# Optimization experiments

Hardware: AMD Instinct MI355X
Metric: run time of the kernel (lower is better)

The kernel has to match this reference:

```python
import jax, jax.numpy as jnp
from jax import lax
import numpy as np

N_STEPS = 5  # hard-coded truncated history length in the module


def setup_inputs() -> dict:
    key = jax.random.key(0)
    kH, kv, k1, k2, k3 = jax.random.split(key, 5)
    B, S, D = 32, 512, 512
    scale = 1.0 / np.sqrt(D)  # keep tanh/softmax out of saturation
    return {
        "H": jax.random.normal(kH, (B, S, D), dtype=jnp.float32),
        "v": jax.random.normal(kv, (D, 1), dtype=jnp.float32) * scale,
        "W1": jax.random.normal(k1, (D, D), dtype=jnp.float32) * scale,
        "W2": jax.random.normal(k2, (D, D), dtype=jnp.float32) * scale,
        "W3": jax.random.normal(k3, (D, D), dtype=jnp.float32) * scale,
    }


def reference(H, v, W1, W2, W3):
    # H: [B, S, D] -> output [B, S, D] (torch returns list of S tensors [B,1,D])
    B, S, D = H.shape

    def step(carry, ht):  # ht: [B, D]
        H_prev, H_prev_tilde = carry  # each [B, N_STEPS, D]
        # temp: [B, N_STEPS, D]; ht @ W2 broadcasts over the history axis
        temp = jnp.tanh(H_prev @ W1 + (ht @ W2)[:, None, :] + H_prev_tilde @ W3)
        w_t = jax.nn.softmax(temp @ v, axis=1)            # [B, N_STEPS, 1]
        ht_hat = jnp.sum(H_prev_tilde * w_t, axis=1)      # [B, D]
        ht_tilde = ht + jax.nn.relu(ht_hat)               # [B, D]
        H_prev = jnp.concatenate([H_prev[:, 1:, :], ht[:, None, :]], axis=1)
        H_prev_tilde = jnp.concatenate([H_prev_tilde[:, 1:, :], ht_tilde[:, None, :]], axis=1)
        return (H_prev, H_prev_tilde), ht_tilde

    init = (jnp.zeros((B, N_STEPS, D), H.dtype), jnp.zeros((B, N_STEPS, D), H.dtype))
    _, ys = lax.scan(step, init, jnp.swapaxes(H, 0, 1))  # ys: [S, B, D]
    return jnp.swapaxes(ys, 0, 1)  # [B, S, D]
```

## Files before the change

kernel.cpp:

```cpp
#include <hip/hip_runtime.h>


#define BB 32
#define SS 512
#define DD 512
#define NS 5

#define A_ELEMS    ((size_t)BB * SS * DD)
#define EXCH_U64_PER_B 128
#define EXCH_OFF   (A_ELEMS * 4)
#define EXCH_BYTES ((size_t)BB * EXCH_U64_PER_B * 8)
#define WS_NEED    (EXCH_OFF + EXCH_BYTES)

typedef __attribute__((ext_vector_type(4))) float f32x4;
typedef __attribute__((ext_vector_type(8))) __bf16 bf16x8;

template <int CTRL, int RMASK, int BMASK, bool BC>
__device__ __forceinline__ float dpp_term(float x) {
  return __uint_as_float((unsigned)__builtin_amdgcn_update_dpp(
      0, (int)__float_as_uint(x), CTRL, RMASK, BMASK, BC));
}
__device__ __forceinline__ float wave_sum64(float x) {
  x += dpp_term<0xB1, 0xF, 0xF, true>(x);
  x += dpp_term<0x4E, 0xF, 0xF, true>(x);
  x += dpp_term<0x141, 0xF, 0xF, true>(x);
  x += dpp_term<0x140, 0xF, 0xF, true>(x);
  x += dpp_term<0x142, 0xA, 0xF, false>(x);
  x += dpp_term<0x143, 0xC, 0xF, false>(x);
  return x;
}
__device__ __forceinline__ float group8_sum(float x) {
  x += dpp_term<0xB1, 0xF, 0xF, true>(x);
  x += dpp_term<0x4E, 0xF, 0xF, true>(x);
  x += dpp_term<0x141, 0xF, 0xF, true>(x);
  return x;
}

__global__ void __launch_bounds__(512) th_phase2(
    const float* __restrict__ H, const float* __restrict__ v,
    const float* __restrict__ W1, const float* __restrict__ W2,
    const float* __restrict__ W3,
    float* __restrict__ A,
    float* __restrict__ Ob,
    unsigned long long* __restrict__ exch) {
  const int tid = threadIdx.x;
  const int b = blockIdx.x & 31;
  const int g = blockIdx.x >> 5;
  const int q = tid >> 6;
  const int ln = tid & 63;
  const int col = (g << 6) + ln;

  __shared__ float tlds[DD];
  __shared__ float pm[DD];
  __shared__ float wl[8];

  const float* Hb = H + (size_t)b * SS * DD;
  float* Ab = A + (size_t)b * SS * DD;
  float* Op = Ob + (size_t)b * SS * DD;
  unsigned long long* eb = exch + (size_t)b * EXCH_U64_PER_B;

  {
    const int lm = ln & 15;
    const int lkb = (ln >> 4) << 3;
    const int lr4 = (ln >> 4) << 2;
#pragma unroll 1
    for (int mat = 0; mat < 2; ++mat) {
      const float* Wm = mat ? W2 : W1;
      float* Out = mat ? Op : Ab;
      f32x4 acc[4][4];
#pragma unroll
      for (int x = 0; x < 4; ++x)
#pragma unroll
        for (int y = 0; y < 4; ++y)
          acc[x][y] = (f32x4){0.f, 0.f, 0.f, 0.f};
#pragma unroll 1
      for (int s = 0; s < 16; ++s) {
        const int kb = s * 32 + lkb;
        bf16x8 af[4];
#pragma unroll
        for (int mt = 0; mt < 4; ++mt) {
          const float* hp = Hb + (size_t)(q * 64 + mt * 16 + lm) * DD + kb;
          float4 u0 = *(const float4*)hp;
          float4 u1 = *(const float4*)(hp + 4);
          bf16x8 t;
          t[0] = (__bf16)u0.x; t[1] = (__bf16)u0.y;
          t[2] = (__bf16)u0.z; t[3] = (__bf16)u0.w;
          t[4] = (__bf16)u1.x; t[5] = (__bf16)u1.y;
          t[6] = (__bf16)u1.z; t[7] = (__bf16)u1.w;
          af[mt] = t;
        }
#pragma unroll
        for (int nt = 0; nt < 4; ++nt) {
          const float* wp = Wm + (size_t)kb * DD + (g * 64 + nt * 16 + lm);
          bf16x8 bfr;
#pragma unroll
          for (int i = 0; i < 8; ++i) bfr[i] = (__bf16)wp[(size_t)i * DD];
#pragma unroll
          for (int mt = 0; mt < 4; ++mt)
            acc[mt][nt] = __builtin_amdgcn_mfma_f32_16x16x32_bf16(
                af[mt], bfr, acc[mt][nt], 0, 0, 0);
        }
      }
#pragma unroll
      for (int mt = 0; mt < 4; ++mt)
#pragma unroll
        for (int nt = 0; nt < 4; ++nt)
#pragma unroll
          for (int i = 0; i < 4; ++i)
            Out[(size_t)(q * 64 + mt * 16 + lr4 + i) * DD +
                (g * 64 + nt * 16 + lm)] = acc[mt][nt][i];
    }
    __syncthreads();
  }

  float wa[64];
#pragma unroll
  for (int i = 0; i < 64; ++i)
    wa[i] = W3[(size_t)(q * 64 + i) * DD + col];

  float v_col = (q < NS) ? v[col] : 0.f;
  float aA[NS] = {0.f, 0.f, 0.f, 0.f, 0.f};
  float cC[NS] = {0.f, 0.f, 0.f, 0.f, 0.f};
  float tl[NS] = {0.f, 0.f, 0.f, 0.f, 0.f};
  float s4_prev = 0.f;
  float tld0 = 0.f;
  float h_cur = Hb[tid];
  float btB = (q < NS) ? Op[DD + col] : 0.f;

  if (tid < NS) wl[tid] = 0.2f;

#pragma unroll 1
  for (int t5 = 0; t5 < 515; t5 += 5) {
#pragma unroll
    for (int p = 0; p < NS; ++p) {
      const int t = t5 + p;
      if (t < SS) {
        const bool pub = (t + 1 < SS);

        float aN_v = 0.f, bt2 = 0.f;
        if (q < NS) {
          aN_v = Ab[(size_t)t * DD + col];
          if (t + 2 < SS) bt2 = Op[(size_t)(t + 2) * DD + col];
        }
        float h_nxt = 0.f;
        if (pub) h_nxt = Hb[(size_t)(t + 1) * DD + tid];

        if (q >= 1 && q < NS && pub) {
          float aa = aA[(p + 1) % NS];
          aa = (q == 2) ? aA[(p + 2) % NS] : aa;
          aa = (q == 3) ? aA[(p + 3) % NS] : aa;
          aa = (q == 4) ? aA[(p + 4) % NS] : aa;
          float cc = cC[(p + 1) % NS];
          cc = (q == 2) ? cC[(p + 2) % NS] : cc;
          cc = (q == 3) ? cC[(p + 3) % NS] : cc;
          cc = (q == 4) ? cC[(p + 4) % NS] : cc;
          float x = aa + btB + cc;
          float e = __expf(2.0f * x);
          float s = (1.0f - 2.0f / (e + 1.0f)) * v_col;
          s = wave_sum64(s);
          if (ln == 63)
            __hip_atomic_store(&eb[(size_t)((t + 1) & 1) * 64 + (q - 1) * 8 + g],
                (unsigned long long)__float_as_uint(s) |
                    ((unsigned long long)(t + 2) << 32),
                __ATOMIC_RELAXED, __HIP_MEMORY_SCOPE_AGENT);
        }

        if (q == 0 && t >= 1) {
          const unsigned long long* wsl = eb + (size_t)(t & 1) * 64;
          float pv = 0.f;
          if (ln < 40) {
            if (!((ln >> 3) == 4 && (ln & 7) == g)) {
              unsigned long long w;
              do {
                w = __hip_atomic_load(&wsl[ln], __ATOMIC_RELAXED,
                                      __HIP_MEMORY_SCOPE_AGENT);
              } while ((unsigned)(w >> 32) != (unsigned)(t + 1));
              pv = __uint_as_float((unsigned)w);
            } else {
              pv = s4_prev;
            }
          }
          pv = group8_sum(pv);
          float sc0 = __shfl(pv, 0, 64);
          float sc1 = __shfl(pv, 8, 64);
          float sc2 = __shfl(pv, 16, 64);
          float sc3 = __shfl(pv, 24, 64);
          float sc4 = __shfl(pv, 32, 64);
          float mx = fmaxf(fmaxf(fmaxf(sc0, sc1), fmaxf(sc2, sc3)), sc4);
          float e0 = __expf(sc0 - mx), e1 = __expf(sc1 - mx);
          float e2 = __expf(sc2 - mx), e3 = __expf(sc3 - mx);
          float e4 = __expf(sc4 - mx);
          float inv = 1.0f / (e0 + e1 + e2 + e3 + e4);
          float wv = e0 * inv;
          wv = (ln == 1) ? e1 * inv : wv;
          wv = (ln == 2) ? e2 * inv : wv;
          wv = (ln == 3) ? e3 * inv : wv;
          wv = (ln == 4) ? e4 * inv : wv;
          if (ln < NS) wl[ln] = wv;
        }
        __syncthreads();

        float w0 = wl[0], w1 = wl[1], w2 = wl[2], w3_ = wl[3], w4 = wl[4];
        float hh = w0 * tl[p];
        hh = fmaf(w1, tl[(p + 1) % NS], hh);
        hh = fmaf(w2, tl[(p + 2) % NS], hh);
        hh = fmaf(w3_, tl[(p + 3) % NS], hh);
        hh = fmaf(w4, tl[(p + 4) % NS], hh);
        float tld = h_cur + fmaxf(hh, 0.f);
        tl[p] = tld;
        tlds[tid] = tld;
        if (g == 0) {
          if (t == 0) {
            tld0 = tld;
          } else {
            Op[(size_t)t * DD + tid] = tld;
            if (t == 1) Op[tid] = tld0;
          }
        }
        asm volatile("s_waitcnt lgkmcnt(0)" ::: "memory");

        float a0 = 0.f, a1 = 0.f, a2 = 0.f, a3 = 0.f;
        const f32x4* tv = (const f32x4*)&tlds[q << 6];
#pragma unroll
        for (int i = 0; i < 16; ++i) {
          f32x4 t4 = tv[i];
          a0 = fmaf(t4.x, wa[4 * i + 0], a0);
          a1 = fmaf(t4.y, wa[4 * i + 1], a1);
          a2 = fmaf(t4.z, wa[4 * i + 2], a2);
          a3 = fmaf(t4.w, wa[4 * i + 3], a3);
        }
        pm[tid] = (a0 + a1) + (a2 + a3);
        __syncthreads();

        if (q < NS) {
          float c = 0.f;
#pragma unroll
          for (int s = 0; s < 8; ++s) c += pm[s * 64 + ln];
          aA[p] = aN_v;
          cC[p] = c;
          if (q == 0 && pub) {
            float x = aN_v + btB + c;
            float e = __expf(2.0f * x);
            float s4 = (1.0f - 2.0f / (e + 1.0f)) * v_col;
            s4 = wave_sum64(s4);
            if (ln == 63)
              __hip_atomic_store(&eb[(size_t)((t + 1) & 1) * 64 + 32 + g],
                  (unsigned long long)__float_as_uint(s4) |
                      ((unsigned long long)(t + 2) << 32),
                  __ATOMIC_RELAXED, __HIP_MEMORY_SCOPE_AGENT);
            s4_prev = __shfl(s4, 63, 64);
          }
          btB = bt2;
        }
        h_cur = h_nxt;
      }
    }
  }
}

extern "C" void kernel_launch(void* const* d_in, const int* in_sizes, int n_in,
                              void* d_out, int out_size, void* d_ws, size_t ws_size,
                              hipStream_t stream) {
  const float* H  = (const float*)d_in[0];
  const float* v  = (const float*)d_in[1];
  const float* W1 = (const float*)d_in[2];
  const float* W2 = (const float*)d_in[3];
  const float* W3 = (const float*)d_in[4];
  float* out = (float*)d_out;

  if (ws_size < WS_NEED) return;

  float* A = (float*)d_ws;
  unsigned long long* exch = (unsigned long long*)((char*)d_ws + EXCH_OFF);

  (void)hipMemsetAsync(exch, 0, EXCH_BYTES, stream);
  hipLaunchKernelGGL(th_phase2, dim3(BB * 8), dim3(512), 0, stream,
                     H, v, W1, W2, W3, A, out, exch);
}
```

Measured before the change: 977.7 us.

## Keep W1/W2 projection slices in LDS as bf16 instead of global workspace

Each block now writes its 512x64 H@W1 and H@W2 projection slices into dynamic shared memory as bf16, replacing the global fp32 workspace and the output buffer it borrowed for staging. The recurrent loop reads these from LDS instead of global memory, and the t==0 output special-case disappears because the output buffer is no longer reused as scratch. This cuts global traffic and per-step load latency in the serial loop. In exchange it uses about 128KB of dynamic LDS and rounds the projections to bf16, which may reduce accuracy.

```diff
diff --git a/kernel.cpp b/kernel.cpp
--- a/kernel.cpp
+++ b/kernel.cpp
@@ -6,11 +6,10 @@
 #define DD 512
 #define NS 5
 
-#define A_ELEMS    ((size_t)BB * SS * DD)
 #define EXCH_U64_PER_B 128
-#define EXCH_OFF   (A_ELEMS * 4)
 #define EXCH_BYTES ((size_t)BB * EXCH_U64_PER_B * 8)
-#define WS_NEED    (EXCH_OFF + EXCH_BYTES)
+#define WS_NEED    EXCH_BYTES
+#define DYN_LDS_BYTES ((size_t)2 * SS * 64 * 2)
 
 typedef __attribute__((ext_vector_type(4))) float f32x4;
 typedef __attribute__((ext_vector_type(8))) __bf16 bf16x8;
@@ -36,11 +35,10 @@
   return x;
 }
 
-__global__ void __launch_bounds__(512) th_phase2(
+__global__ void __launch_bounds__(512) th_fused(
     const float* __restrict__ H, const float* __restrict__ v,
     const float* __restrict__ W1, const float* __restrict__ W2,
     const float* __restrict__ W3,
-    float* __restrict__ A,
     float* __restrict__ Ob,
     unsigned long long* __restrict__ exch) {
   const int tid = threadIdx.x;
@@ -53,9 +51,11 @@
   __shared__ float tlds[DD];
   __shared__ float pm[DD];
   __shared__ float wl[8];
+  extern __shared__ __align__(16) unsigned char dynls[];
+  __bf16* aS = (__bf16*)dynls;
+  __bf16* bS = aS + (size_t)SS * 64;
 
   const float* Hb = H + (size_t)b * SS * DD;
-  float* Ab = A + (size_t)b * SS * DD;
   float* Op = Ob + (size_t)b * SS * DD;
   unsigned long long* eb = exch + (size_t)b * EXCH_U64_PER_B;
 
@@ -66,7 +66,7 @@
 #pragma unroll 1
     for (int mat = 0; mat < 2; ++mat) {
       const float* Wm = mat ? W2 : W1;
-      float* Out = mat ? Op : Ab;
+      __bf16* Out = mat ? bS : aS;
       f32x4 acc[4][4];
 #pragma unroll
       for (int x = 0; x < 4; ++x)
@@ -107,8 +107,8 @@
         for (int nt = 0; nt < 4; ++nt)
 #pragma unroll
           for (int i = 0; i < 4; ++i)
-            Out[(size_t)(q * 64 + mt * 16 + lr4 + i) * DD +
-                (g * 64 + nt * 16 + lm)] = acc[mt][nt][i];
+            Out[(size_t)(q * 64 + mt * 16 + lr4 + i) * 64 + nt * 16 + lm] =
+                (__bf16)acc[mt][nt][i];
     }
     __syncthreads();
   }
@@ -123,9 +123,8 @@
   float cC[NS] = {0.f, 0.f, 0.f, 0.f, 0.f};
   float tl[NS] = {0.f, 0.f, 0.f, 0.f, 0.f};
   float s4_prev = 0.f;
-  float tld0 = 0.f;
   float h_cur = Hb[tid];
-  float btB = (q < NS) ? Op[DD + col] : 0.f;
+  float btB = (q < NS) ? (float)bS[64 + ln] : 0.f;
 
   if (tid < NS) wl[tid] = 0.2f;
 
@@ -139,8 +138,8 @@
 
         float aN_v = 0.f, bt2 = 0.f;
         if (q < NS) {
-          aN_v = Ab[(size_t)t * DD + col];
-          if (t + 2 < SS) bt2 = Op[(size_t)(t + 2) * DD + col];
+          aN_v = (float)aS[(size_t)t * 64 + ln];
+          if (t + 2 < SS) bt2 = (float)bS[(size_t)(t + 2) * 64 + ln];
         }
         float h_nxt = 0.f;
         if (pub) h_nxt = Hb[(size_t)(t + 1) * DD + tid];
@@ -209,14 +208,7 @@
         float tld = h_cur + fmaxf(hh, 0.f);
         tl[p] = tld;
         tlds[tid] = tld;
-        if (g == 0) {
-          if (t == 0) {
-            tld0 = tld;
-          } else {
-            Op[(size_t)t * DD + tid] = tld;
-            if (t == 1) Op[tid] = tld0;
-          }
-        }
+        if (g == 0) Op[(size_t)t * DD + tid] = tld;
         asm volatile("s_waitcnt lgkmcnt(0)" ::: "memory");
 
         float a0 = 0.f, a1 = 0.f, a2 = 0.f, a3 = 0.f;
@@ -270,10 +262,9 @@
 
   if (ws_size < WS_NEED) return;
 
-  float* A = (float*)d_ws;
-  unsigned long long* exch = (unsigned long long*)((char*)d_ws + EXCH_OFF);
+  unsigned long long* exch = (unsigned long long*)d_ws;
 
   (void)hipMemsetAsync(exch, 0, EXCH_BYTES, stream);
-  hipLaunchKernelGGL(th_phase2, dim3(BB * 8), dim3(512), 0, stream,
-                     H, v, W1, W2, W3, A, out, exch);
-}
+  hipLaunchKernelGGL(th_fused, dim3(BB * 8), dim3(512), DYN_LDS_BYTES, stream,
+                     H, v, W1, W2, W3, out, exch);
+}
```

Measured after the change: 926.5 us, median of 2. 1.06x faster.
